# Kernel tuning notes

Measured on AMD Instinct MI355X. Metric: run time of the kernel, lower is better.

Reference implementation:

```python
import jax, jax.numpy as jnp
import numpy as np

EMB_DIM = 256
ATTN_DIM = 64
B, K = 16384, 64


def setup_inputs() -> dict:
    key = jax.random.key(0)
    ks = jax.random.split(key, 7)
    center = jax.random.normal(ks[0], (B, EMB_DIM), dtype=jnp.float32)
    neigh_embs = jax.random.normal(ks[1], (B, K, EMB_DIM), dtype=jnp.float32)
    ppi_weights = jax.random.uniform(ks[2], (B, K), dtype=jnp.float32)
    # learned params (Linear stores weight as [out, in]; we keep that layout)
    Wq = jax.random.normal(ks[3], (ATTN_DIM, EMB_DIM), dtype=jnp.float32) / np.sqrt(EMB_DIM)
    Wk = jax.random.normal(ks[4], (ATTN_DIM, EMB_DIM), dtype=jnp.float32) / np.sqrt(EMB_DIM)
    # xavier_uniform for W_gate: limit = sqrt(6/(fan_in+fan_out))
    lim = np.sqrt(6.0 / (2 * EMB_DIM + EMB_DIM))
    Wgate = jax.random.uniform(ks[5], (EMB_DIM, 2 * EMB_DIM), minval=-lim, maxval=lim, dtype=jnp.float32)
    bgate = jnp.zeros((EMB_DIM,), dtype=jnp.float32)
    return {"center": center, "neigh_embs": neigh_embs, "ppi_weights": ppi_weights,
            "Wq": Wq, "Wk": Wk, "Wgate": Wgate, "bgate": bgate}


def reference(center, neigh_embs, ppi_weights, Wq, Wk, Wgate, bgate):
    scale = ATTN_DIM ** -0.5
    q = center @ Wq.T                                   # [B, a]
    k = jnp.einsum('bkd,ad->bka', neigh_embs, Wk)        # [B, K, a]
    logits = jnp.einsum('ba,bka->bk', q, k) * scale      # [B, K]
    attn = jax.nn.softmax(logits, axis=-1)
    attn = attn * ppi_weights
    attn = attn / (jnp.sum(attn, axis=-1, keepdims=True) + 1e-8)
    # dropout is identity in eval mode
    context = jnp.einsum('bk,bkd->bd', attn, neigh_embs)  # [B, D]
    gate = jax.nn.sigmoid(jnp.concatenate([center, context], axis=-1) @ Wgate.T + bgate)
    return gate * center + (1.0 - gate) * context
```

## Files before the change

kernel.cpp:

```cpp
#include <hip/hip_runtime.h>
#include <hip/hip_bf16.h>
#include <cstdint>

#define B_N 16384
#define KN 64
#define DN 256
#define AN 64
#define ROWS 4

typedef float f32x4 __attribute__((ext_vector_type(4)));
typedef float f32x2 __attribute__((ext_vector_type(2)));
typedef short s16x8 __attribute__((ext_vector_type(8)));

static __device__ inline unsigned int pk2(float a, float b) {
    __hip_bfloat162 h = __float22bfloat162_rn(make_float2(a, b));
    return *reinterpret_cast<unsigned int*>(&h);
}
static __device__ inline float bf_lo(unsigned int v) { return __uint_as_float(v << 16); }
static __device__ inline float bf_hi(unsigned int v) { return __uint_as_float(v & 0xFFFF0000u); }

__global__ __launch_bounds__(256) void prep_kernel(const float* __restrict__ Wq,
                                                   const float* __restrict__ Wk,
                                                   const float* __restrict__ Wgate,
                                                   float* __restrict__ M,
                                                   unsigned int* __restrict__ Wgb) {
    int blk = blockIdx.x;
    int t = threadIdx.x;
    if (blk < DN) {
        float acc = 0.f;
        #pragma unroll
        for (int a = 0; a < AN; ++a)
            acc += Wq[a * DN + blk] * Wk[a * DN + t];
        M[blk * DN + t] = acc;
    } else {
        int d = blk - DN;
        const float* src = Wgate + (size_t)d * (2 * DN);
        Wgb[(size_t)d * 256 + t] = pk2(src[2 * t], src[2 * t + 1]);
    }
}

__global__ __launch_bounds__(256, 2) void attn_kernel(const float* __restrict__ neigh,
                                                      const float* __restrict__ center,
                                                      const float* __restrict__ ppi,
                                                      const float* __restrict__ M,
                                                      float* __restrict__ ctx) {
    __shared__ unsigned int sn[KN * 128];
    __shared__ unsigned int sqk[ROWS * 128];
    __shared__ float slog[KN];
    __shared__ float sattn[KN];
    __shared__ float scr[DN];

    const int tid = threadIdx.x;
    const int lane = tid & 63;
    const int b0 = blockIdx.x * ROWS;

    f32x4 rr[16];
    {
        const f32x4* t4 = (const f32x4*)(neigh + (size_t)b0 * (KN * DN));
        #pragma unroll
        for (int i = 0; i < 16; ++i)
            rr[i] = __builtin_nontemporal_load(t4 + tid + 256 * i);
    }

    float pv[ROWS];
    #pragma unroll
    for (int r = 0; r < ROWS; ++r) pv[r] = ppi[(size_t)(b0 + r) * KN + lane];

    {
        float qa[ROWS] = {0.f, 0.f, 0.f, 0.f};
        const float* cp = center + (size_t)b0 * DN;
        #pragma unroll 8
        for (int i = 0; i < DN; ++i) {
            float mv = M[(size_t)i * DN + tid];
            qa[0] += cp[i] * mv;
            qa[1] += cp[DN + i] * mv;
            qa[2] += cp[2 * DN + i] * mv;
            qa[3] += cp[3 * DN + i] * mv;
        }
        #pragma unroll
        for (int r = 0; r < ROWS; ++r) {
            float other = __shfl_xor(qa[r], 1, 64);
            if ((tid & 1) == 0)
                sqk[r * 128 + (tid >> 1)] = pk2(qa[r], other);
        }
    }

    #pragma unroll
    for (int r = 0; r < ROWS; ++r) {
        if (r > 0) __syncthreads();

        {
            uint2* dst = (uint2*)sn;
            #pragma unroll
            for (int i = 0; i < 16; ++i)
                dst[tid + 256 * i] = make_uint2(pk2(rr[i].x, rr[i].y), pk2(rr[i].z, rr[i].w));
        }
        if (r < ROWS - 1) {
            const f32x4* n4 = (const f32x4*)(neigh + (size_t)(b0 + r + 1) * (KN * DN));
            #pragma unroll
            for (int i = 0; i < 16; ++i)
                rr[i] = __builtin_nontemporal_load(n4 + tid + 256 * i);
        }
        __syncthreads();

        {
            const int g = tid >> 2, j = tid & 3;
            float acc = 0.f;
            #pragma unroll
            for (int m = 0; m < 32; ++m) {
                int s = (m + g) & 31;
                int p = j + 4 * s;
                unsigned int nv = sn[g * 128 + p];
                unsigned int qv = sqk[r * 128 + p];
                acc += bf_lo(nv) * bf_lo(qv) + bf_hi(nv) * bf_hi(qv);
            }
            acc += __shfl_xor(acc, 1, 64);
            acc += __shfl_xor(acc, 2, 64);
            if (j == 0) slog[g] = acc;
        }
        __syncthreads();

        if (tid < KN) {
            float l = slog[tid] * 0.125f;
            float mx = l;
            #pragma unroll
            for (int off = 32; off >= 1; off >>= 1)
                mx = fmaxf(mx, __shfl_xor(mx, off, 64));
            float e = expf(l - mx);
            float se = e;
            #pragma unroll
            for (int off = 32; off >= 1; off >>= 1)
                se += __shfl_xor(se, off, 64);
            float pr = e / se;
            float t = pr * pv[r];
            float st = t;
            #pragma unroll
            for (int off = 32; off >= 1; off >>= 1)
                st += __shfl_xor(st, off, 64);
            sattn[tid] = t / (st + 1e-8f);
        }
        __syncthreads();

        {
            const int p = tid & 127, h = tid >> 7;
            float c0 = 0.f, c1 = 0.f;
            #pragma unroll
            for (int kk = 0; kk < 32; ++kk) {
                int k = h * 32 + kk;
                unsigned int nv = sn[k * 128 + p];
                float a = sattn[k];
                c0 += a * bf_lo(nv);
                c1 += a * bf_hi(nv);
            }
            if (h == 1) ((float2*)scr)[p] = make_float2(c0, c1);
            __syncthreads();
            if (h == 0) {
                float2 o = ((float2*)scr)[p];
                f32x2 res = {o.x + c0, o.y + c1};
                __builtin_nontemporal_store(res, (f32x2*)(ctx + (size_t)(b0 + r) * DN) + p);
            }
        }
    }
}

__global__ __launch_bounds__(256) void gate_kernel(const float* __restrict__ center,
                                                   const float* __restrict__ ctxw,
                                                   const unsigned int* __restrict__ Wgb,
                                                   const float* __restrict__ bgate,
                                                   float* __restrict__ out) {
    __shared__ unsigned int xsb[32 * 260];
    const int r0 = blockIdx.x * 32;
    const int tid = threadIdx.x;

    const float4* c4 = (const float4*)(center + (size_t)r0 * DN);
    const float4* x4 = (const float4*)(ctxw + (size_t)r0 * DN);
    #pragma unroll
    for (int i = 0; i < 8; ++i) {
        int idx = tid + 256 * i;
        int r = idx >> 6, c = idx & 63;
        float4 cv = c4[idx];
        float4 xv = x4[idx];
        *(uint2*)&xsb[r * 260 + 2 * c]       = make_uint2(pk2(cv.x, cv.y), pk2(cv.z, cv.w));
        *(uint2*)&xsb[r * 260 + 128 + 2 * c] = make_uint2(pk2(xv.x, xv.y), pk2(xv.z, xv.w));
    }
    __syncthreads();

    const int wave = tid >> 6, lane = tid & 63;
    const int l15 = lane & 15, lhi = lane >> 4;

    f32x4 acc[2][4];
    #pragma unroll
    for (int mt = 0; mt < 2; ++mt)
        #pragma unroll
        for (int nt = 0; nt < 4; ++nt)
            acc[mt][nt] = (f32x4){0.f, 0.f, 0.f, 0.f};

    #pragma unroll
    for (int ks = 0; ks < 16; ++ks) {
        s16x8 a0 = *(const s16x8*)&xsb[(l15)      * 260 + ks * 16 + lhi * 4];
        s16x8 a1 = *(const s16x8*)&xsb[(l15 + 16) * 260 + ks * 16 + lhi * 4];
        s16x8 b[4];
        #pragma unroll
        for (int nt = 0; nt < 4; ++nt) {
            int d = wave * 64 + nt * 16 + l15;
            b[nt] = *(const s16x8*)&Wgb[(size_t)d * 256 + ks * 16 + lhi * 4];
        }
        #pragma unroll
        for (int nt = 0; nt < 4; ++nt) {
            acc[0][nt] = __builtin_amdgcn_mfma_f32_16x16x32_bf16(a0, b[nt], acc[0][nt], 0, 0, 0);
            acc[1][nt] = __builtin_amdgcn_mfma_f32_16x16x32_bf16(a1, b[nt], acc[1][nt], 0, 0, 0);
        }
    }

    #pragma unroll
    for (int mt = 0; mt < 2; ++mt)
        #pragma unroll
        for (int nt = 0; nt < 4; ++nt) {
            int col = wave * 64 + nt * 16 + l15;
            float bg = bgate[col];
            #pragma unroll
            for (int reg = 0; reg < 4; ++reg) {
                int row = mt * 16 + lhi * 4 + reg;
                size_t gr = (size_t)(r0 + row);
                float z = acc[mt][nt][reg] + bg;
                float gt = 1.0f / (1.0f + expf(-z));
                float ce = center[gr * DN + col];
                float cx = ctxw[gr * DN + col];
                out[gr * DN + col] = gt * ce + (1.0f - gt) * cx;
            }
        }
}

extern "C" void kernel_launch(void* const* d_in, const int* in_sizes, int n_in,
                              void* d_out, int out_size, void* d_ws, size_t ws_size,
                              hipStream_t stream) {
    const float* center = (const float*)d_in[0];
    const float* neigh  = (const float*)d_in[1];
    const float* ppi    = (const float*)d_in[2];
    const float* Wq     = (const float*)d_in[3];
    const float* Wk     = (const float*)d_in[4];
    const float* Wgate  = (const float*)d_in[5];
    const float* bgate  = (const float*)d_in[6];
    float* out = (float*)d_out;

    char* ws = (char*)d_ws;
    float* M          = (float*)(ws);
    unsigned int* Wgb = (unsigned int*)(ws + 262144);
    float* ctx        = (float*)(ws + 524288);

    prep_kernel<<<dim3(512), dim3(256), 0, stream>>>(Wq, Wk, Wgate, M, Wgb);
    attn_kernel<<<dim3(B_N / ROWS), dim3(256), 0, stream>>>(neigh, center, ppi, M, ctx);
    gate_kernel<<<dim3(B_N / 32), dim3(256), 0, stream>>>(center, ctx, Wgb, bgate, out);
}
```

Measured before the change: 291.0 us.

## Move query-key projection into a separate register-tiled GEMM kernel

Computes center·M for all rows in a new qk_kernel that tiles 32 rows in shared memory with 4x8 register blocking, and stores the result as bf16. The attention kernel now just loads these precomputed vectors instead of streaming the whole M matrix per block of 4 rows. Its launch bounds go from 2 to 4 blocks per CU so more blocks can hide memory latency. The cost is an extra kernel launch, an 8 MB intermediate round trip through memory, and possible register spills under the tighter occupancy bound.

```diff
diff --git a/kernel.cpp b/kernel.cpp
--- a/kernel.cpp
+++ b/kernel.cpp
@@ -39,10 +39,61 @@
     }
 }
 
-__global__ __launch_bounds__(256, 2) void attn_kernel(const float* __restrict__ neigh,
-                                                      const float* __restrict__ center,
+__global__ __launch_bounds__(256) void qk_kernel(const float* __restrict__ center,
+                                                 const float* __restrict__ M,
+                                                 unsigned int* __restrict__ qkb) {
+    __shared__ float xs[32 * DN];
+    int r0 = blockIdx.x * 32;
+    int tid = threadIdx.x;
+
+    const float4* src = (const float4*)(center + (size_t)r0 * DN);
+    float4* dst = (float4*)xs;
+    #pragma unroll
+    for (int i = 0; i < 8; ++i)
+        dst[tid + 256 * i] = src[tid + 256 * i];
+    __syncthreads();
+
+    int ty = tid >> 5, tx = tid & 31;
+    float acc[4][8];
+    #pragma unroll
+    for (int r = 0; r < 4; ++r)
+        #pragma unroll
+        for (int c = 0; c < 8; ++c) acc[r][c] = 0.f;
+
+    for (int k4 = 0; k4 < DN; k4 += 4) {
+        float4 xr[4];
+        #pragma unroll
+        for (int r = 0; r < 4; ++r)
+            xr[r] = *(const float4*)(&xs[(ty * 4 + r) * DN + k4]);
+        #pragma unroll
+        for (int kk = 0; kk < 4; ++kk) {
+            float4 ma = *(const float4*)(&M[(size_t)(k4 + kk) * DN + tx * 8]);
+            float4 mb = *(const float4*)(&M[(size_t)(k4 + kk) * DN + tx * 8 + 4]);
+            #pragma unroll
+            for (int r = 0; r < 4; ++r) {
+                float x = (&xr[r].x)[kk];
+                acc[r][0] += x * ma.x; acc[r][1] += x * ma.y;
+                acc[r][2] += x * ma.z; acc[r][3] += x * ma.w;
+                acc[r][4] += x * mb.x; acc[r][5] += x * mb.y;
+                acc[r][6] += x * mb.z; acc[r][7] += x * mb.w;
+            }
+        }
+    }
+    #pragma unroll
+    for (int r = 0; r < 4; ++r) {
+        size_t row = (size_t)(r0 + ty * 4 + r);
+        uint4 o;
+        o.x = pk2(acc[r][0], acc[r][1]);
+        o.y = pk2(acc[r][2], acc[r][3]);
+        o.z = pk2(acc[r][4], acc[r][5]);
+        o.w = pk2(acc[r][6], acc[r][7]);
+        *(uint4*)&qkb[row * 128 + tx * 4] = o;
+    }
+}
+
+__global__ __launch_bounds__(256, 4) void attn_kernel(const float* __restrict__ neigh,
+                                                      const unsigned int* __restrict__ qkb,
                                                       const float* __restrict__ ppi,
-                                                      const float* __restrict__ M,
                                                       float* __restrict__ ctx) {
     __shared__ unsigned int sn[KN * 128];
     __shared__ unsigned int sqk[ROWS * 128];
@@ -62,28 +113,11 @@
             rr[i] = __builtin_nontemporal_load(t4 + tid + 256 * i);
     }
 
+    ((uint2*)sqk)[tid] = ((const uint2*)(qkb + (size_t)b0 * 128))[tid];
+
     float pv[ROWS];
     #pragma unroll
     for (int r = 0; r < ROWS; ++r) pv[r] = ppi[(size_t)(b0 + r) * KN + lane];
-
-    {
-        float qa[ROWS] = {0.f, 0.f, 0.f, 0.f};
-        const float* cp = center + (size_t)b0 * DN;
-        #pragma unroll 8
-        for (int i = 0; i < DN; ++i) {
-            float mv = M[(size_t)i * DN + tid];
-            qa[0] += cp[i] * mv;
-            qa[1] += cp[DN + i] * mv;
-            qa[2] += cp[2 * DN + i] * mv;
-            qa[3] += cp[3 * DN + i] * mv;
-        }
-        #pragma unroll
-        for (int r = 0; r < ROWS; ++r) {
-            float other = __shfl_xor(qa[r], 1, 64);
-            if ((tid & 1) == 0)
-                sqk[r * 128 + (tid >> 1)] = pk2(qa[r], other);
-        }
-    }
 
     #pragma unroll
     for (int r = 0; r < ROWS; ++r) {
@@ -246,9 +280,11 @@
     char* ws = (char*)d_ws;
     float* M          = (float*)(ws);
     unsigned int* Wgb = (unsigned int*)(ws + 262144);
-    float* ctx        = (float*)(ws + 524288);
+    unsigned int* qkb = (unsigned int*)(ws + 524288);
+    float* ctx        = (float*)(ws + 524288 + 8388608);
 
     prep_kernel<<<dim3(512), dim3(256), 0, stream>>>(Wq, Wk, Wgate, M, Wgb);
-    attn_kernel<<<dim3(B_N / ROWS), dim3(256), 0, stream>>>(neigh, center, ppi, M, ctx);
+    qk_kernel<<<dim3(B_N / 32), dim3(256), 0, stream>>>(center, M, qkb);
+    attn_kernel<<<dim3(B_N / ROWS), dim3(256), 0, stream>>>(neigh, qkb, ppi, ctx);
     gate_kernel<<<dim3(B_N / 32), dim3(256), 0, stream>>>(center, ctx, Wgb, bgate, out);
 }
```

After: 529.9 us. 1.82x slower.
